# Kernel tuning notes

Measured on AMD Instinct MI355X. Metric: run time of the kernel, lower is better.

## Reference

```python
import jax, jax.numpy as jnp
import numpy as np

LMAX, RB, RA, N, D = 4, 12, 11, 131072, 64
S = (LMAX + 1) ** 2


def _assoc_legendre_norm(lmax, x):
    # Fully-normalized associated Legendre P_l^m(x), orthonormal over the sphere
    # (includes sqrt((2l+1)/(4pi) * (l-m)!/(l+m)!)). x: [B] = cos(beta).
    B = x.shape[0]
    s = np.sqrt(np.clip(1.0 - x * x, 0.0, 1.0))
    P = np.zeros((lmax + 1, lmax + 1, B))
    P[0, 0] = np.sqrt(1.0 / (4.0 * np.pi))
    for m in range(1, lmax + 1):
        P[m, m] = -np.sqrt((2.0 * m + 1.0) / (2.0 * m)) * s * P[m - 1, m - 1]
    for m in range(0, lmax):
        P[m + 1, m] = np.sqrt(2.0 * m + 3.0) * x * P[m, m]
    for m in range(0, lmax + 1):
        for l in range(m + 2, lmax + 1):
            a = np.sqrt((4.0 * l * l - 1.0) / (l * l - m * m))
            b = np.sqrt((((l - 1) ** 2 - m * m)) / (4.0 * (l - 1) ** 2 - 1.0))
            P[l, m] = a * (x * P[l - 1, m] - b * P[l - 2, m])
    return P


def _sh_grid(lmax, res_beta, res_alpha):
    # Real orthonormal spherical harmonics sampled on a Gauss-Legendre x uniform-alpha grid,
    # plus quadrature weights so that sum_{b,a} Y_i Y_j qw_b = delta_ij (band-limited).
    x, w = np.polynomial.legendre.leggauss(res_beta)  # nodes in cos(beta)
    alpha = 2.0 * np.pi * np.arange(res_alpha) / res_alpha
    P = _assoc_legendre_norm(lmax, x)  # [L+1, L+1, RB]
    Ssz = (lmax + 1) ** 2
    Y = np.zeros((res_beta, res_alpha, Ssz))
    i = 0
    for l in range(lmax + 1):
        for m in range(-l, l + 1):
            if m < 0:
                ang = np.sqrt(2.0) * np.sin(-m * alpha)
            elif m == 0:
                ang = np.ones_like(alpha)
            else:
                ang = np.sqrt(2.0) * np.cos(m * alpha)
            Y[:, :, i] = P[l, abs(m)][:, None] * ang[None, :]
            i += 1
    qw = w * (2.0 * np.pi / res_alpha)  # beta quadrature * alpha trapezoid weight
    return Y.astype(np.float32), qw.astype(np.float32)


def setup_inputs() -> dict:
    key = jax.random.key(0)
    k1, k2, k3, k4 = jax.random.split(key, 4)
    Y_np, qw_np = _sh_grid(LMAX, RB, RA)
    Y = jnp.asarray(Y_np)                       # [RB, RA, S]
    Yw = Y * jnp.asarray(qw_np)[:, None, None]  # [RB, RA, S] (quadrature-weighted)
    input1 = jax.random.normal(k1, (N, D), dtype=jnp.float32)
    input2 = jax.random.normal(k2, (N, D), dtype=jnp.float32)
    W1 = jax.random.normal(k3, (D, S), dtype=jnp.float32) * 0.1
    W2 = jax.random.normal(k4, (D, S), dtype=jnp.float32) * 0.1
    return {"input1": input1, "input2": input2, "W1": W1, "W2": W2, "Y": Y, "Yw": Yw}


def reference(input1, input2, W1, W2, Y, Yw):
    # linear_in: project input irreps to S2 spherical-harmonic coefficients
    c1 = input1 @ W1  # [N, S]
    c2 = input2 @ W2  # [N, S]
    # ToS2Grid: evaluate band-limited signal on the (beta, alpha) grid
    g1 = jnp.einsum("ns,bas->nba", c1, Y)  # [N, RB, RA]
    g2 = jnp.einsum("ns,bas->nba", c2, Y)
    # pointwise product on the sphere, then FromS2Grid (quadrature projection)
    return jnp.einsum("nba,bas->ns", g1 * g2, Yw)  # [N, S]
```

## Files before the change

### kernel.cpp

```cpp
#include <hip/hip_runtime.h>


typedef _Float16 f16x8 __attribute__((ext_vector_type(8)));
typedef _Float16 f16x4 __attribute__((ext_vector_type(4)));
typedef float f32x4 __attribute__((ext_vector_type(4)));
typedef float f32x4u __attribute__((ext_vector_type(4), aligned(4)));

namespace {
constexpr int kD = 64, kS = 25, kP = 132;
constexpr int kBlock = 256, kM = 256;
constexpr int kYfOff = 0;
constexpr int kYwOff = 4608;
constexpr int kLdsHalfs = 9216;
}

__device__ __forceinline__ f16x4 ld4(const _Float16* p) {
    return *reinterpret_cast<const f16x4*>(p);
}
__device__ __forceinline__ f16x8 cvt8h(f32x4 u, f32x4 v) {
    f16x8 r;
    r[0] = (_Float16)u[0]; r[1] = (_Float16)u[1];
    r[2] = (_Float16)u[2]; r[3] = (_Float16)u[3];
    r[4] = (_Float16)v[0]; r[5] = (_Float16)v[1];
    r[6] = (_Float16)v[2]; r[7] = (_Float16)v[3];
    return r;
}

__global__ __launch_bounds__(kBlock, 2) void gaunt_fused9(
    const float* __restrict__ in1, const float* __restrict__ in2,
    const float* __restrict__ W1, const float* __restrict__ W2,
    const float* __restrict__ Y,  const float* __restrict__ Yw,
    float* __restrict__ out)
{
    __shared__ _Float16 lds[kLdsHalfs];
    const int tid  = threadIdx.x;
    const int lane = tid & 63;
    const int w    = __builtin_amdgcn_readfirstlane(tid >> 6);
    const int lo16 = lane & 15, quad = lane >> 4;

    const long long base = (long long)blockIdx.x * (kM * kD);
    f32x4 u1[4][2], v1[4][2], u2[4][2], v2[4][2];
    #pragma unroll
    for (int rt = 0; rt < 4; ++rt) {
        const int row = (4 * w + rt) * 16 + lo16;
        const float* p1 = in1 + base + row * kD + quad * 8;
        const float* p2 = in2 + base + row * kD + quad * 8;
        #pragma unroll
        for (int ks = 0; ks < 2; ++ks) {
            u1[rt][ks] = *reinterpret_cast<const f32x4*>(p1 + ks * 32);
            v1[rt][ks] = *reinterpret_cast<const f32x4*>(p1 + ks * 32 + 4);
            u2[rt][ks] = *reinterpret_cast<const f32x4*>(p2 + ks * 32);
            v2[rt][ks] = *reinterpret_cast<const f32x4*>(p2 + ks * 32 + 4);
        }
    }

    for (int e = tid; e < 4608; e += kBlock) {
        const int i = e & 3, ln = (e >> 2) & 63, r = e >> 8;
        const int pt = r >> 1, st = r & 1;
        const int p = pt * 16 + (ln & 15);
        const int s = st * 16 + ((ln >> 4) & 3) * 4 + i;
        lds[kYfOff + e] = (s < kS && p < kP) ? (_Float16)Y[p * kS + s]
                                             : (_Float16)0.f;
    }
    for (int e = tid; e < 4608; e += kBlock) {
        const int i = e & 3, ln = (e >> 2) & 63, r = e >> 8;
        const int pt = r % 9, st = r / 9;
        const int p = pt * 16 + ((ln >> 4) & 3) * 4 + i;
        const int s = st * 16 + (ln & 15);
        lds[kYwOff + e] = (s < kS && p < kP) ? (_Float16)Yw[p * kS + s]
                                             : (_Float16)0.f;
    }

    f16x8 w1f[2][2], w2f[2][2];
    #pragma unroll
    for (int st = 0; st < 2; ++st) {
        const int s = st * 16 + lo16;
        #pragma unroll
        for (int ks = 0; ks < 2; ++ks) {
            f16x8 a, b;
            #pragma unroll
            for (int j = 0; j < 8; ++j) { a[j] = (_Float16)0.f; b[j] = (_Float16)0.f; }
            if (s < kS) {
                const int d0 = ks * 32 + quad * 8;
                #pragma unroll
                for (int j = 0; j < 8; ++j) {
                    a[j] = (_Float16)W1[(d0 + j) * kS + s];
                    b[j] = (_Float16)W2[(d0 + j) * kS + s];
                }
            }
            w1f[st][ks] = a; w2f[st][ks] = b;
        }
    }

    __syncthreads();

    f16x8 b1[4][2], b2[4][2];
    #pragma unroll
    for (int rt = 0; rt < 4; ++rt)
        #pragma unroll
        for (int ks = 0; ks < 2; ++ks) {
            b1[rt][ks] = cvt8h(u1[rt][ks], v1[rt][ks]);
            b2[rt][ks] = cvt8h(u2[rt][ks], v2[rt][ks]);
        }

    f16x4 h1c[4][2], h2c[4][2];
    #pragma unroll
    for (int rt = 0; rt < 4; ++rt) {
        #pragma unroll
        for (int st = 0; st < 2; ++st) {
            f32x4 c1 = (f32x4){0.f, 0.f, 0.f, 0.f};
            f32x4 c2 = (f32x4){0.f, 0.f, 0.f, 0.f};
            #pragma unroll
            for (int ks = 0; ks < 2; ++ks) {
                c1 = __builtin_amdgcn_mfma_f32_16x16x32_f16(w1f[st][ks], b1[rt][ks], c1, 0, 0, 0);
                c2 = __builtin_amdgcn_mfma_f32_16x16x32_f16(w2f[st][ks], b2[rt][ks], c2, 0, 0, 0);
            }
            f16x4 hc1, hc2;
            #pragma unroll
            for (int i = 0; i < 4; ++i) {
                hc1[i] = (_Float16)c1[i];
                hc2[i] = (_Float16)c2[i];
            }
            h1c[rt][st] = hc1; h2c[rt][st] = hc2;
        }
    }

    f32x4 oacc[4][2];
    #pragma unroll
    for (int rt = 0; rt < 4; ++rt)
        #pragma unroll
        for (int st = 0; st < 2; ++st)
            oacc[rt][st] = (f32x4){0.f, 0.f, 0.f, 0.f};

    f16x4 yfc[2], yw0c, yw1c;
    yfc[0] = ld4(&lds[kYfOff + (0 * 2 + 0) * 256 + lane * 4]);
    yfc[1] = ld4(&lds[kYfOff + (0 * 2 + 1) * 256 + lane * 4]);
    yw0c   = ld4(&lds[kYwOff + (0 * 9 + 0) * 256 + lane * 4]);
    yw1c   = ld4(&lds[kYwOff + (1 * 9 + 0) * 256 + lane * 4]);

    #pragma unroll 1
    for (int pt = 0; pt < 9; ++pt) {
        f16x4 yfn[2], yw0n, yw1n;
        if (pt < 8) {
            yfn[0] = ld4(&lds[kYfOff + ((pt + 1) * 2 + 0) * 256 + lane * 4]);
            yfn[1] = ld4(&lds[kYfOff + ((pt + 1) * 2 + 1) * 256 + lane * 4]);
            yw0n   = ld4(&lds[kYwOff + (0 * 9 + pt + 1) * 256 + lane * 4]);
            yw1n   = ld4(&lds[kYwOff + (1 * 9 + pt + 1) * 256 + lane * 4]);
        }
        #pragma unroll
        for (int rt = 0; rt < 4; ++rt) {
            const f32x4 z = (f32x4){0.f, 0.f, 0.f, 0.f};
            f32x4 g1 = __builtin_amdgcn_mfma_f32_16x16x16f16(yfc[0], h1c[rt][0], z, 0, 0, 0);
            g1       = __builtin_amdgcn_mfma_f32_16x16x16f16(yfc[1], h1c[rt][1], g1, 0, 0, 0);
            f32x4 g2 = __builtin_amdgcn_mfma_f32_16x16x16f16(yfc[0], h2c[rt][0], z, 0, 0, 0);
            g2       = __builtin_amdgcn_mfma_f32_16x16x16f16(yfc[1], h2c[rt][1], g2, 0, 0, 0);
            f16x4 h;
            h[0] = (_Float16)(g1[0] * g2[0]);
            h[1] = (_Float16)(g1[1] * g2[1]);
            h[2] = (_Float16)(g1[2] * g2[2]);
            h[3] = (_Float16)(g1[3] * g2[3]);
            oacc[rt][0] = __builtin_amdgcn_mfma_f32_16x16x16f16(yw0c, h, oacc[rt][0], 0, 0, 0);
            oacc[rt][1] = __builtin_amdgcn_mfma_f32_16x16x16f16(yw1c, h, oacc[rt][1], 0, 0, 0);
        }
        yfc[0] = yfn[0]; yfc[1] = yfn[1]; yw0c = yw0n; yw1c = yw1n;
    }

    const long long ob = (long long)blockIdx.x * (kM * kS);
    #pragma unroll
    for (int rt = 0; rt < 4; ++rt) {
        const int row = (4 * w + rt) * 16 + lo16;
        float* rp = out + ob + (long long)row * kS;
        *reinterpret_cast<f32x4u*>(rp + quad * 4) = oacc[rt][0];
        if (quad < 2) {
            *reinterpret_cast<f32x4u*>(rp + 16 + quad * 4) = oacc[rt][1];
        } else if (quad == 2) {
            rp[24] = oacc[rt][1][0];
        }
    }
}

extern "C" void kernel_launch(void* const* d_in, const int* in_sizes, int n_in,
                              void* d_out, int out_size, void* d_ws, size_t ws_size,
                              hipStream_t stream) {
    const float* in1 = (const float*)d_in[0];
    const float* in2 = (const float*)d_in[1];
    const float* W1  = (const float*)d_in[2];
    const float* W2  = (const float*)d_in[3];
    const float* Y   = (const float*)d_in[4];
    const float* Yw  = (const float*)d_in[5];
    float* out = (float*)d_out;
    (void)d_ws; (void)ws_size;

    const int n_rows = in_sizes[0] / kD;
    const int grid = n_rows / kM;
    gaunt_fused9<<<grid, kBlock, 0, stream>>>(in1, in2, W1, W2, Y, Yw, out);
}
```

Before: 115.8 us.

## Process two row tiles per block and prefetch the second during compute

Each block now handles two 256-row tiles. The Y/Yw LDS tables and W fragments are built once and reused for both tiles. Global loads for the second tile are issued before the first tile is computed, so load latency overlaps with MFMA work. The grid is halved to 256 blocks and launch bounds are relaxed to one block per SM, which allows more registers but lowers occupancy and leaves fewer blocks than before to spread across the CUs.

```diff
diff --git a/kernel.cpp b/kernel.cpp
--- a/kernel.cpp
+++ b/kernel.cpp
@@ -26,7 +26,7 @@
     return r;
 }
 
-__global__ __launch_bounds__(kBlock, 2) void gaunt_fused9(
+__global__ __launch_bounds__(kBlock, 1) void gaunt_fused10(
     const float* __restrict__ in1, const float* __restrict__ in2,
     const float* __restrict__ W1, const float* __restrict__ W2,
     const float* __restrict__ Y,  const float* __restrict__ Yw,
@@ -38,21 +38,27 @@
     const int w    = __builtin_amdgcn_readfirstlane(tid >> 6);
     const int lo16 = lane & 15, quad = lane >> 4;
 
-    const long long base = (long long)blockIdx.x * (kM * kD);
-    f32x4 u1[4][2], v1[4][2], u2[4][2], v2[4][2];
-    #pragma unroll
-    for (int rt = 0; rt < 4; ++rt) {
-        const int row = (4 * w + rt) * 16 + lo16;
-        const float* p1 = in1 + base + row * kD + quad * 8;
-        const float* p2 = in2 + base + row * kD + quad * 8;
-        #pragma unroll
-        for (int ks = 0; ks < 2; ++ks) {
-            u1[rt][ks] = *reinterpret_cast<const f32x4*>(p1 + ks * 32);
-            v1[rt][ks] = *reinterpret_cast<const f32x4*>(p1 + ks * 32 + 4);
-            u2[rt][ks] = *reinterpret_cast<const f32x4*>(p2 + ks * 32);
-            v2[rt][ks] = *reinterpret_cast<const f32x4*>(p2 + ks * 32 + 4);
-        }
-    }
+    const long long rowbase = (long long)blockIdx.x * (2 * kM);
+
+    f32x4 su1[4][2], sv1[4][2], su2[4][2], sv2[4][2];
+
+    auto issue_loads = [&](long long rb) {
+        #pragma unroll
+        for (int rt = 0; rt < 4; ++rt) {
+            const long long row = rb + (4 * w + rt) * 16 + lo16;
+            const float* p1 = in1 + row * kD + quad * 8;
+            const float* p2 = in2 + row * kD + quad * 8;
+            #pragma unroll
+            for (int ks = 0; ks < 2; ++ks) {
+                su1[rt][ks] = *reinterpret_cast<const f32x4*>(p1 + ks * 32);
+                sv1[rt][ks] = *reinterpret_cast<const f32x4*>(p1 + ks * 32 + 4);
+                su2[rt][ks] = *reinterpret_cast<const f32x4*>(p2 + ks * 32);
+                sv2[rt][ks] = *reinterpret_cast<const f32x4*>(p2 + ks * 32 + 4);
+            }
+        }
+    };
+
+    issue_loads(rowbase);
 
     for (int e = tid; e < 4608; e += kBlock) {
         const int i = e & 3, ln = (e >> 2) & 63, r = e >> 8;
@@ -95,88 +101,98 @@
     __syncthreads();
 
     f16x8 b1[4][2], b2[4][2];
-    #pragma unroll
-    for (int rt = 0; rt < 4; ++rt)
-        #pragma unroll
-        for (int ks = 0; ks < 2; ++ks) {
-            b1[rt][ks] = cvt8h(u1[rt][ks], v1[rt][ks]);
-            b2[rt][ks] = cvt8h(u2[rt][ks], v2[rt][ks]);
-        }
-
-    f16x4 h1c[4][2], h2c[4][2];
-    #pragma unroll
-    for (int rt = 0; rt < 4; ++rt) {
-        #pragma unroll
-        for (int st = 0; st < 2; ++st) {
-            f32x4 c1 = (f32x4){0.f, 0.f, 0.f, 0.f};
-            f32x4 c2 = (f32x4){0.f, 0.f, 0.f, 0.f};
+    auto cvt_all = [&]() {
+        #pragma unroll
+        for (int rt = 0; rt < 4; ++rt)
             #pragma unroll
             for (int ks = 0; ks < 2; ++ks) {
-                c1 = __builtin_amdgcn_mfma_f32_16x16x32_f16(w1f[st][ks], b1[rt][ks], c1, 0, 0, 0);
-                c2 = __builtin_amdgcn_mfma_f32_16x16x32_f16(w2f[st][ks], b2[rt][ks], c2, 0, 0, 0);
-            }
-            f16x4 hc1, hc2;
-            #pragma unroll
-            for (int i = 0; i < 4; ++i) {
-                hc1[i] = (_Float16)c1[i];
-                hc2[i] = (_Float16)c2[i];
-            }
-            h1c[rt][st] = hc1; h2c[rt][st] = hc2;
-        }
-    }
-
-    f32x4 oacc[4][2];
-    #pragma unroll
-    for (int rt = 0; rt < 4; ++rt)
-        #pragma unroll
-        for (int st = 0; st < 2; ++st)
-            oacc[rt][st] = (f32x4){0.f, 0.f, 0.f, 0.f};
-
-    f16x4 yfc[2], yw0c, yw1c;
-    yfc[0] = ld4(&lds[kYfOff + (0 * 2 + 0) * 256 + lane * 4]);
-    yfc[1] = ld4(&lds[kYfOff + (0 * 2 + 1) * 256 + lane * 4]);
-    yw0c   = ld4(&lds[kYwOff + (0 * 9 + 0) * 256 + lane * 4]);
-    yw1c   = ld4(&lds[kYwOff + (1 * 9 + 0) * 256 + lane * 4]);
-
-    #pragma unroll 1
-    for (int pt = 0; pt < 9; ++pt) {
-        f16x4 yfn[2], yw0n, yw1n;
-        if (pt < 8) {
-            yfn[0] = ld4(&lds[kYfOff + ((pt + 1) * 2 + 0) * 256 + lane * 4]);
-            yfn[1] = ld4(&lds[kYfOff + ((pt + 1) * 2 + 1) * 256 + lane * 4]);
-            yw0n   = ld4(&lds[kYwOff + (0 * 9 + pt + 1) * 256 + lane * 4]);
-            yw1n   = ld4(&lds[kYwOff + (1 * 9 + pt + 1) * 256 + lane * 4]);
-        }
+                b1[rt][ks] = cvt8h(su1[rt][ks], sv1[rt][ks]);
+                b2[rt][ks] = cvt8h(su2[rt][ks], sv2[rt][ks]);
+            }
+    };
+
+    auto compute_store = [&](long long rb) {
+        f16x4 h1c[4][2], h2c[4][2];
         #pragma unroll
         for (int rt = 0; rt < 4; ++rt) {
-            const f32x4 z = (f32x4){0.f, 0.f, 0.f, 0.f};
-            f32x4 g1 = __builtin_amdgcn_mfma_f32_16x16x16f16(yfc[0], h1c[rt][0], z, 0, 0, 0);
-            g1       = __builtin_amdgcn_mfma_f32_16x16x16f16(yfc[1], h1c[rt][1], g1, 0, 0, 0);
-            f32x4 g2 = __builtin_amdgcn_mfma_f32_16x16x16f16(yfc[0], h2c[rt][0], z, 0, 0, 0);
-            g2       = __builtin_amdgcn_mfma_f32_16x16x16f16(yfc[1], h2c[rt][1], g2, 0, 0, 0);
-            f16x4 h;
-            h[0] = (_Float16)(g1[0] * g2[0]);
-            h[1] = (_Float16)(g1[1] * g2[1]);
-            h[2] = (_Float16)(g1[2] * g2[2]);
-            h[3] = (_Float16)(g1[3] * g2[3]);
-            oacc[rt][0] = __builtin_amdgcn_mfma_f32_16x16x16f16(yw0c, h, oacc[rt][0], 0, 0, 0);
-            oacc[rt][1] = __builtin_amdgcn_mfma_f32_16x16x16f16(yw1c, h, oacc[rt][1], 0, 0, 0);
-        }
-        yfc[0] = yfn[0]; yfc[1] = yfn[1]; yw0c = yw0n; yw1c = yw1n;
-    }
-
-    const long long ob = (long long)blockIdx.x * (kM * kS);
-    #pragma unroll
-    for (int rt = 0; rt < 4; ++rt) {
-        const int row = (4 * w + rt) * 16 + lo16;
-        float* rp = out + ob + (long long)row * kS;
-        *reinterpret_cast<f32x4u*>(rp + quad * 4) = oacc[rt][0];
-        if (quad < 2) {
-            *reinterpret_cast<f32x4u*>(rp + 16 + quad * 4) = oacc[rt][1];
-        } else if (quad == 2) {
-            rp[24] = oacc[rt][1][0];
-        }
-    }
+            #pragma unroll
+            for (int st = 0; st < 2; ++st) {
+                f32x4 c1 = (f32x4){0.f, 0.f, 0.f, 0.f};
+                f32x4 c2 = (f32x4){0.f, 0.f, 0.f, 0.f};
+                #pragma unroll
+                for (int ks = 0; ks < 2; ++ks) {
+                    c1 = __builtin_amdgcn_mfma_f32_16x16x32_f16(w1f[st][ks], b1[rt][ks], c1, 0, 0, 0);
+                    c2 = __builtin_amdgcn_mfma_f32_16x16x32_f16(w2f[st][ks], b2[rt][ks], c2, 0, 0, 0);
+                }
+                f16x4 hc1, hc2;
+                #pragma unroll
+                for (int i = 0; i < 4; ++i) {
+                    hc1[i] = (_Float16)c1[i];
+                    hc2[i] = (_Float16)c2[i];
+                }
+                h1c[rt][st] = hc1; h2c[rt][st] = hc2;
+            }
+        }
+
+        f32x4 oacc[4][2];
+        #pragma unroll
+        for (int rt = 0; rt < 4; ++rt)
+            #pragma unroll
+            for (int st = 0; st < 2; ++st)
+                oacc[rt][st] = (f32x4){0.f, 0.f, 0.f, 0.f};
+
+        f16x4 yfc[2], yw0c, yw1c;
+        yfc[0] = ld4(&lds[kYfOff + 0 * 256 + lane * 4]);
+        yfc[1] = ld4(&lds[kYfOff + 1 * 256 + lane * 4]);
+        yw0c   = ld4(&lds[kYwOff + 0 * 256 + lane * 4]);
+        yw1c   = ld4(&lds[kYwOff + 9 * 256 + lane * 4]);
+
+        #pragma unroll 1
+        for (int pt = 0; pt < 9; ++pt) {
+            f16x4 yfn[2], yw0n, yw1n;
+            if (pt < 8) {
+                yfn[0] = ld4(&lds[kYfOff + ((pt + 1) * 2 + 0) * 256 + lane * 4]);
+                yfn[1] = ld4(&lds[kYfOff + ((pt + 1) * 2 + 1) * 256 + lane * 4]);
+                yw0n   = ld4(&lds[kYwOff + (0 * 9 + pt + 1) * 256 + lane * 4]);
+                yw1n   = ld4(&lds[kYwOff + (1 * 9 + pt + 1) * 256 + lane * 4]);
+            }
+            #pragma unroll
+            for (int rt = 0; rt < 4; ++rt) {
+                const f32x4 z = (f32x4){0.f, 0.f, 0.f, 0.f};
+                f32x4 g1 = __builtin_amdgcn_mfma_f32_16x16x16f16(yfc[0], h1c[rt][0], z, 0, 0, 0);
+                g1       = __builtin_amdgcn_mfma_f32_16x16x16f16(yfc[1], h1c[rt][1], g1, 0, 0, 0);
+                f32x4 g2 = __builtin_amdgcn_mfma_f32_16x16x16f16(yfc[0], h2c[rt][0], z, 0, 0, 0);
+                g2       = __builtin_amdgcn_mfma_f32_16x16x16f16(yfc[1], h2c[rt][1], g2, 0, 0, 0);
+                f16x4 h;
+                h[0] = (_Float16)(g1[0] * g2[0]);
+                h[1] = (_Float16)(g1[1] * g2[1]);
+                h[2] = (_Float16)(g1[2] * g2[2]);
+                h[3] = (_Float16)(g1[3] * g2[3]);
+                oacc[rt][0] = __builtin_amdgcn_mfma_f32_16x16x16f16(yw0c, h, oacc[rt][0], 0, 0, 0);
+                oacc[rt][1] = __builtin_amdgcn_mfma_f32_16x16x16f16(yw1c, h, oacc[rt][1], 0, 0, 0);
+            }
+            yfc[0] = yfn[0]; yfc[1] = yfn[1]; yw0c = yw0n; yw1c = yw1n;
+        }
+
+        #pragma unroll
+        for (int rt = 0; rt < 4; ++rt) {
+            const long long row = rb + (4 * w + rt) * 16 + lo16;
+            float* rp = out + row * kS;
+            *reinterpret_cast<f32x4u*>(rp + quad * 4) = oacc[rt][0];
+            if (quad < 2) {
+                *reinterpret_cast<f32x4u*>(rp + 16 + quad * 4) = oacc[rt][1];
+            } else if (quad == 2) {
+                rp[24] = oacc[rt][1][0];
+            }
+        }
+    };
+
+    cvt_all();
+    issue_loads(rowbase + kM);
+    compute_store(rowbase);
+
+    cvt_all();
+    compute_store(rowbase + kM);
 }
 
 extern "C" void kernel_launch(void* const* d_in, const int* in_sizes, int n_in,
@@ -192,6 +208,6 @@
     (void)d_ws; (void)ws_size;
 
     const int n_rows = in_sizes[0] / kD;
-    const int grid = n_rows / kM;
-    gaunt_fused9<<<grid, kBlock, 0, stream>>>(in1, in2, W1, W2, Y, Yw, out);
-}
+    const int grid = n_rows / (2 * kM);
+    gaunt_fused10<<<grid, kBlock, 0, stream>>>(in1, in2, W1, W2, Y, Yw, out);
+}
```

After: 117.3 us. About the same (+1.3%).

## Precompute fp16 MFMA fragments in a prologue kernel and stream inputs via LDS DMA

Applied to the files above, without the earlier changes.

Adds a small prologue kernel that converts Y, Yw and the weight matrices into fp16 MFMA fragment layouts in workspace, so the main kernel reads them directly from global memory instead of rebuilding them per block. The main kernel shrinks each block to 64 rows (one row tile per wave), allows 4 blocks per CU, and loads the input rows into swizzled LDS with global_load_lds DMA. This cuts per-block setup cost and register pressure and raises occupancy. In exchange it adds a second launch and per-iteration global reads of the Y fragments in place of LDS reads.

```diff
diff --git a/kernel.cpp b/kernel.cpp
--- a/kernel.cpp
+++ b/kernel.cpp
@@ -8,12 +8,48 @@
 
 namespace {
 constexpr int kD = 64, kS = 25, kP = 132;
-constexpr int kBlock = 256, kM = 256;
+constexpr int kBlock = 256, kM = 64;
 constexpr int kYfOff = 0;
 constexpr int kYwOff = 4608;
-constexpr int kLdsHalfs = 9216;
-}
-
+constexpr int kWfOff = 9216;
+constexpr int kWsHalfs = 13312;
+}
+
+__global__ void precompute11(const float* __restrict__ W1,
+                             const float* __restrict__ W2,
+                             const float* __restrict__ Y,
+                             const float* __restrict__ Yw,
+                             _Float16* __restrict__ ws) {
+    const int e = blockIdx.x * blockDim.x + threadIdx.x;
+    if (e < 4608) {
+        const int i = e & 3, ln = (e >> 2) & 63, r = e >> 8;
+        const int pt = r >> 1, st = r & 1;
+        const int p = pt * 16 + (ln & 15);
+        const int s = st * 16 + ((ln >> 4) & 3) * 4 + i;
+        ws[kYfOff + e] = (s < kS && p < kP) ? (_Float16)Y[p * kS + s]
+                                            : (_Float16)0.f;
+    } else if (e < 9216) {
+        const int e2 = e - 4608;
+        const int i = e2 & 3, ln = (e2 >> 2) & 63, r = e2 >> 8;
+        const int pt = r % 9, st = r / 9;
+        const int p = pt * 16 + ((ln >> 4) & 3) * 4 + i;
+        const int s = st * 16 + (ln & 15);
+        ws[kYwOff + e2] = (s < kS && p < kP) ? (_Float16)Yw[p * kS + s]
+                                             : (_Float16)0.f;
+    } else if (e < kWsHalfs) {
+        const int e3 = e - 9216;
+        const int j = e3 & 7, ln = (e3 >> 3) & 63, r = e3 >> 9;
+        const int ks = r & 1, st = (r >> 1) & 1, op = r >> 2;
+        const int s = st * 16 + (ln & 15);
+        const int d = ks * 32 + ((ln >> 4) & 3) * 8 + j;
+        const float* W = op ? W2 : W1;
+        ws[kWfOff + e3] = (s < kS) ? (_Float16)W[d * kS + s] : (_Float16)0.f;
+    }
+}
+
+__device__ __forceinline__ f16x8 ld8(const _Float16* p) {
+    return *reinterpret_cast<const f16x8*>(p);
+}
 __device__ __forceinline__ f16x4 ld4(const _Float16* p) {
     return *reinterpret_cast<const f16x4*>(p);
 }
@@ -26,156 +62,124 @@
     return r;
 }
 
-__global__ __launch_bounds__(kBlock, 2) void gaunt_fused9(
+__global__ __launch_bounds__(kBlock, 4) void gaunt_fused11(
     const float* __restrict__ in1, const float* __restrict__ in2,
-    const float* __restrict__ W1, const float* __restrict__ W2,
-    const float* __restrict__ Y,  const float* __restrict__ Yw,
-    float* __restrict__ out)
+    const _Float16* __restrict__ ws, float* __restrict__ out)
 {
-    __shared__ _Float16 lds[kLdsHalfs];
+    __shared__ f32x4 ldsq[2][kM][16];
+
     const int tid  = threadIdx.x;
     const int lane = tid & 63;
     const int w    = __builtin_amdgcn_readfirstlane(tid >> 6);
     const int lo16 = lane & 15, quad = lane >> 4;
 
-    const long long base = (long long)blockIdx.x * (kM * kD);
-    f32x4 u1[4][2], v1[4][2], u2[4][2], v2[4][2];
-    #pragma unroll
-    for (int rt = 0; rt < 4; ++rt) {
-        const int row = (4 * w + rt) * 16 + lo16;
-        const float* p1 = in1 + base + row * kD + quad * 8;
-        const float* p2 = in2 + base + row * kD + quad * 8;
+    const long long rowbase = (long long)blockIdx.x * kM;
+
+    {
+        const int rg = lane >> 4;
+        const int sl = lane & 15;
+        #pragma unroll
+        for (int i = 0; i < 8; ++i) {
+            const int t  = w * 8 + i;
+            const int op = t >> 4, q = t & 15;
+            const int r  = q * 4 + rg;
+            const int c16 = sl ^ (r & 7);
+            const float* src = (op ? in2 : in1) + (rowbase + r) * kD + c16 * 4;
+            char* dst = (char*)(&ldsq[0][0][0]) + op * 16384 + q * 1024;
+            __builtin_amdgcn_global_load_lds(
+                (const __attribute__((address_space(1))) void*)src,
+                (__attribute__((address_space(3))) void*)dst,
+                16, 0, 0);
+        }
+    }
+
+    const _Float16* wsYf = ws + kYfOff;
+    const _Float16* wsYw = ws + kYwOff;
+    const _Float16* wsWf = ws + kWfOff;
+
+    f16x8 w1f[2][2], w2f[2][2];
+    #pragma unroll
+    for (int st = 0; st < 2; ++st)
         #pragma unroll
         for (int ks = 0; ks < 2; ++ks) {
-            u1[rt][ks] = *reinterpret_cast<const f32x4*>(p1 + ks * 32);
-            v1[rt][ks] = *reinterpret_cast<const f32x4*>(p1 + ks * 32 + 4);
-            u2[rt][ks] = *reinterpret_cast<const f32x4*>(p2 + ks * 32);
-            v2[rt][ks] = *reinterpret_cast<const f32x4*>(p2 + ks * 32 + 4);
-        }
-    }
-
-    for (int e = tid; e < 4608; e += kBlock) {
-        const int i = e & 3, ln = (e >> 2) & 63, r = e >> 8;
-        const int pt = r >> 1, st = r & 1;
-        const int p = pt * 16 + (ln & 15);
-        const int s = st * 16 + ((ln >> 4) & 3) * 4 + i;
-        lds[kYfOff + e] = (s < kS && p < kP) ? (_Float16)Y[p * kS + s]
-                                             : (_Float16)0.f;
-    }
-    for (int e = tid; e < 4608; e += kBlock) {
-        const int i = e & 3, ln = (e >> 2) & 63, r = e >> 8;
-        const int pt = r % 9, st = r / 9;
-        const int p = pt * 16 + ((ln >> 4) & 3) * 4 + i;
-        const int s = st * 16 + (ln & 15);
-        lds[kYwOff + e] = (s < kS && p < kP) ? (_Float16)Yw[p * kS + s]
-                                             : (_Float16)0.f;
-    }
-
-    f16x8 w1f[2][2], w2f[2][2];
+            w1f[st][ks] = ld8(&wsWf[((0 * 2 + st) * 2 + ks) * 512 + lane * 8]);
+            w2f[st][ks] = ld8(&wsWf[((1 * 2 + st) * 2 + ks) * 512 + lane * 8]);
+        }
+    f16x4 yfc0 = ld4(&wsYf[0 * 256 + lane * 4]);
+    f16x4 yfc1 = ld4(&wsYf[1 * 256 + lane * 4]);
+    f16x4 yw0c = ld4(&wsYw[0 * 256 + lane * 4]);
+    f16x4 yw1c = ld4(&wsYw[9 * 256 + lane * 4]);
+
+    __syncthreads();
+
+    const int r  = w * 16 + lo16;
+    const int r7 = lo16 & 7;
+    f16x8 b1[2], b2[2];
+    #pragma unroll
+    for (int ks = 0; ks < 2; ++ks) {
+        const int s0 = ks * 8 + quad * 2;
+        const f32x4 u = ldsq[0][r][s0 ^ r7];
+        const f32x4 v = ldsq[0][r][(s0 + 1) ^ r7];
+        b1[ks] = cvt8h(u, v);
+    }
+    #pragma unroll
+    for (int ks = 0; ks < 2; ++ks) {
+        const int s0 = ks * 8 + quad * 2;
+        const f32x4 u = ldsq[1][r][s0 ^ r7];
+        const f32x4 v = ldsq[1][r][(s0 + 1) ^ r7];
+        b2[ks] = cvt8h(u, v);
+    }
+
+    f16x4 h1c[2], h2c[2];
     #pragma unroll
     for (int st = 0; st < 2; ++st) {
-        const int s = st * 16 + lo16;
+        f32x4 c1 = (f32x4){0.f, 0.f, 0.f, 0.f};
+        f32x4 c2 = (f32x4){0.f, 0.f, 0.f, 0.f};
         #pragma unroll
         for (int ks = 0; ks < 2; ++ks) {
-            f16x8 a, b;
-            #pragma unroll
-            for (int j = 0; j < 8; ++j) { a[j] = (_Float16)0.f; b[j] = (_Float16)0.f; }
-            if (s < kS) {
-                const int d0 = ks * 32 + quad * 8;
-                #pragma unroll
-                for (int j = 0; j < 8; ++j) {
-                    a[j] = (_Float16)W1[(d0 + j) * kS + s];
-                    b[j] = (_Float16)W2[(d0 + j) * kS + s];
-                }
-            }
-            w1f[st][ks] = a; w2f[st][ks] = b;
-        }
-    }
-
-    __syncthreads();
-
-    f16x8 b1[4][2], b2[4][2];
-    #pragma unroll
-    for (int rt = 0; rt < 4; ++rt)
-        #pragma unroll
-        for (int ks = 0; ks < 2; ++ks) {
-            b1[rt][ks] = cvt8h(u1[rt][ks], v1[rt][ks]);
-            b2[rt][ks] = cvt8h(u2[rt][ks], v2[rt][ks]);
-        }
-
-    f16x4 h1c[4][2], h2c[4][2];
-    #pragma unroll
-    for (int rt = 0; rt < 4; ++rt) {
-        #pragma unroll
-        for (int st = 0; st < 2; ++st) {
-            f32x4 c1 = (f32x4){0.f, 0.f, 0.f, 0.f};
-            f32x4 c2 = (f32x4){0.f, 0.f, 0.f, 0.f};
-            #pragma unroll
-            for (int ks = 0; ks < 2; ++ks) {
-                c1 = __builtin_amdgcn_mfma_f32_16x16x32_f16(w1f[st][ks], b1[rt][ks], c1, 0, 0, 0);
-                c2 = __builtin_amdgcn_mfma_f32_16x16x32_f16(w2f[st][ks], b2[rt][ks], c2, 0, 0, 0);
-            }
-            f16x4 hc1, hc2;
-            #pragma unroll
-            for (int i = 0; i < 4; ++i) {
-                hc1[i] = (_Float16)c1[i];
-                hc2[i] = (_Float16)c2[i];
-            }
-            h1c[rt][st] = hc1; h2c[rt][st] = hc2;
-        }
-    }
-
-    f32x4 oacc[4][2];
-    #pragma unroll
-    for (int rt = 0; rt < 4; ++rt)
-        #pragma unroll
-        for (int st = 0; st < 2; ++st)
-            oacc[rt][st] = (f32x4){0.f, 0.f, 0.f, 0.f};
-
-    f16x4 yfc[2], yw0c, yw1c;
-    yfc[0] = ld4(&lds[kYfOff + (0 * 2 + 0) * 256 + lane * 4]);
-    yfc[1] = ld4(&lds[kYfOff + (0 * 2 + 1) * 256 + lane * 4]);
-    yw0c   = ld4(&lds[kYwOff + (0 * 9 + 0) * 256 + lane * 4]);
-    yw1c   = ld4(&lds[kYwOff + (1 * 9 + 0) * 256 + lane * 4]);
+            c1 = __builtin_amdgcn_mfma_f32_16x16x32_f16(w1f[st][ks], b1[ks], c1, 0, 0, 0);
+            c2 = __builtin_amdgcn_mfma_f32_16x16x32_f16(w2f[st][ks], b2[ks], c2, 0, 0, 0);
+        }
+        #pragma unroll
+        for (int i = 0; i < 4; ++i) {
+            h1c[st][i] = (_Float16)c1[i];
+            h2c[st][i] = (_Float16)c2[i];
+        }
+    }
+
+    f32x4 oacc0 = (f32x4){0.f, 0.f, 0.f, 0.f};
+    f32x4 oacc1 = (f32x4){0.f, 0.f, 0.f, 0.f};
 
     #pragma unroll 1
     for (int pt = 0; pt < 9; ++pt) {
-        f16x4 yfn[2], yw0n, yw1n;
+        f16x4 yfn0, yfn1, yw0n, yw1n;
         if (pt < 8) {
-            yfn[0] = ld4(&lds[kYfOff + ((pt + 1) * 2 + 0) * 256 + lane * 4]);
-            yfn[1] = ld4(&lds[kYfOff + ((pt + 1) * 2 + 1) * 256 + lane * 4]);
-            yw0n   = ld4(&lds[kYwOff + (0 * 9 + pt + 1) * 256 + lane * 4]);
-            yw1n   = ld4(&lds[kYwOff + (1 * 9 + pt + 1) * 256 + lane * 4]);
-        }
-        #pragma unroll
-        for (int rt = 0; rt < 4; ++rt) {
-            const f32x4 z = (f32x4){0.f, 0.f, 0.f, 0.f};
-            f32x4 g1 = __builtin_amdgcn_mfma_f32_16x16x16f16(yfc[0], h1c[rt][0], z, 0, 0, 0);
-            g1       = __builtin_amdgcn_mfma_f32_16x16x16f16(yfc[1], h1c[rt][1], g1, 0, 0, 0);
-            f32x4 g2 = __builtin_amdgcn_mfma_f32_16x16x16f16(yfc[0], h2c[rt][0], z, 0, 0, 0);
-            g2       = __builtin_amdgcn_mfma_f32_16x16x16f16(yfc[1], h2c[rt][1], g2, 0, 0, 0);
-            f16x4 h;
-            h[0] = (_Float16)(g1[0] * g2[0]);
-            h[1] = (_Float16)(g1[1] * g2[1]);
-            h[2] = (_Float16)(g1[2] * g2[2]);
-            h[3] = (_Float16)(g1[3] * g2[3]);
-            oacc[rt][0] = __builtin_amdgcn_mfma_f32_16x16x16f16(yw0c, h, oacc[rt][0], 0, 0, 0);
-            oacc[rt][1] = __builtin_amdgcn_mfma_f32_16x16x16f16(yw1c, h, oacc[rt][1], 0, 0, 0);
-        }
-        yfc[0] = yfn[0]; yfc[1] = yfn[1]; yw0c = yw0n; yw1c = yw1n;
-    }
-
-    const long long ob = (long long)blockIdx.x * (kM * kS);
-    #pragma unroll
-    for (int rt = 0; rt < 4; ++rt) {
-        const int row = (4 * w + rt) * 16 + lo16;
-        float* rp = out + ob + (long long)row * kS;
-        *reinterpret_cast<f32x4u*>(rp + quad * 4) = oacc[rt][0];
-        if (quad < 2) {
-            *reinterpret_cast<f32x4u*>(rp + 16 + quad * 4) = oacc[rt][1];
-        } else if (quad == 2) {
-            rp[24] = oacc[rt][1][0];
-        }
+            yfn0 = ld4(&wsYf[((pt + 1) * 2 + 0) * 256 + lane * 4]);
+            yfn1 = ld4(&wsYf[((pt + 1) * 2 + 1) * 256 + lane * 4]);
+            yw0n = ld4(&wsYw[(0 * 9 + pt + 1) * 256 + lane * 4]);
+            yw1n = ld4(&wsYw[(1 * 9 + pt + 1) * 256 + lane * 4]);
+        }
+        const f32x4 z = (f32x4){0.f, 0.f, 0.f, 0.f};
+        f32x4 g1 = __builtin_amdgcn_mfma_f32_16x16x16f16(yfc0, h1c[0], z, 0, 0, 0);
+        g1       = __builtin_amdgcn_mfma_f32_16x16x16f16(yfc1, h1c[1], g1, 0, 0, 0);
+        f32x4 g2 = __builtin_amdgcn_mfma_f32_16x16x16f16(yfc0, h2c[0], z, 0, 0, 0);
+        g2       = __builtin_amdgcn_mfma_f32_16x16x16f16(yfc1, h2c[1], g2, 0, 0, 0);
+        f16x4 h;
+        h[0] = (_Float16)(g1[0] * g2[0]);
+        h[1] = (_Float16)(g1[1] * g2[1]);
+        h[2] = (_Float16)(g1[2] * g2[2]);
+        h[3] = (_Float16)(g1[3] * g2[3]);
+        oacc0 = __builtin_amdgcn_mfma_f32_16x16x16f16(yw0c, h, oacc0, 0, 0, 0);
+        oacc1 = __builtin_amdgcn_mfma_f32_16x16x16f16(yw1c, h, oacc1, 0, 0, 0);
+        yfc0 = yfn0; yfc1 = yfn1; yw0c = yw0n; yw1c = yw1n;
+    }
+
+    float* rp = out + (rowbase + r) * kS;
+    *reinterpret_cast<f32x4u*>(rp + quad * 4) = oacc0;
+    if (quad < 2) {
+        *reinterpret_cast<f32x4u*>(rp + 16 + quad * 4) = oacc1;
+    } else if (quad == 2) {
+        rp[24] = oacc1[0];
     }
 }
 
@@ -189,9 +193,11 @@
     const float* Y   = (const float*)d_in[4];
     const float* Yw  = (const float*)d_in[5];
     float* out = (float*)d_out;
-    (void)d_ws; (void)ws_size;
+    _Float16* ws = (_Float16*)d_ws;
+
+    precompute11<<<52, 256, 0, stream>>>(W1, W2, Y, Yw, ws);
 
     const int n_rows = in_sizes[0] / kD;
     const int grid = n_rows / kM;
-    gaunt_fused9<<<grid, kBlock, 0, stream>>>(in1, in2, W1, W2, Y, Yw, out);
-}
+    gaunt_fused11<<<grid, kBlock, 0, stream>>>(in1, in2, ws, out);
+}
```

After: 112.6 us. -2.7%, faster.
